# Kernel tuning notes

Hardware: AMD Instinct MI355X
Metric: run time of the kernel (lower is better)

The kernel has to match this reference:

```python
import jax, jax.numpy as jnp
import numpy as np

B, T, NE = 2, 2048, 1024
NH, NKV, HD = 16, 4, 64
GC = 32  # ve_gate_channels
WIN = 1024  # sliding window (left)
EPS = 1e-6


def rope(x, cos, sin):
    # x: (B,T,H,D), cos/sin: (B,T,D//2)
    cos = cos[:, :, None, :]
    sin = sin[:, :, None, :]
    x1, x2 = jnp.split(x, 2, axis=-1)
    return jnp.concatenate([x1 * cos + x2 * sin, -x1 * sin + x2 * cos], axis=-1)


def rmsnorm(x):
    return x * jax.lax.rsqrt(jnp.mean(x * x, axis=-1, keepdims=True) + EPS)


def setup_inputs() -> dict:
    key = jax.random.key(0)
    ks = jax.random.split(key, 7)
    x = jax.random.normal(ks[0], (B, T, NE), jnp.float32)
    ve = jax.random.normal(ks[1], (B, T, NKV * HD), jnp.float32)
    # real RoPE tables (already 'sliced to correct positions')
    inv_freq = 1.0 / (10000.0 ** (jnp.arange(HD // 2, dtype=jnp.float32) / (HD // 2)))
    ang = jnp.arange(T, dtype=jnp.float32)[:, None] * inv_freq[None, :]  # (T, D//2)
    cos = jnp.broadcast_to(jnp.cos(ang)[None], (B, T, HD // 2))
    sin = jnp.broadcast_to(jnp.sin(ang)[None], (B, T, HD // 2))
    s = 0.02
    Wq = jax.random.normal(ks[2], (NE, NH * HD), jnp.float32) * s
    Wk = jax.random.normal(ks[3], (NE, NKV * HD), jnp.float32) * s
    Wv = jax.random.normal(ks[4], (NE, NKV * HD), jnp.float32) * s
    Wo = jax.random.normal(ks[5], (NE, NE), jnp.float32) * s
    Wg = jax.random.normal(ks[6], (GC, NKV), jnp.float32) * s
    return {"x": x, "ve": ve, "cos": cos, "sin": sin,
            "Wq": Wq, "Wk": Wk, "Wv": Wv, "Wo": Wo, "Wg": Wg,
            "window_size": WIN}


def reference(x, ve, cos, sin, Wq, Wk, Wv, Wo, Wg, window_size):
    Bs, Ts, _ = x.shape
    q = (x @ Wq).reshape(Bs, Ts, NH, HD)
    k = (x @ Wk).reshape(Bs, Ts, NKV, HD)
    v = (x @ Wv).reshape(Bs, Ts, NKV, HD)
    # gated value embeddings
    gate = 2.0 * jax.nn.sigmoid(x[..., :GC] @ Wg)  # (B,T,NKV)
    v = v + gate[..., None] * ve.reshape(Bs, Ts, NKV, HD)
    q = rmsnorm(rope(q, cos, sin))
    k = rmsnorm(rope(k, cos, sin))
    # GQA: head h uses kv head h // rep
    rep = NH // NKV
    k = jnp.repeat(k, rep, axis=2)
    v = jnp.repeat(v, rep, axis=2)
    scale = 1.0 / jnp.sqrt(jnp.float32(HD))
    scores = jnp.einsum('bthd,bshd->bhts', q, k) * scale  # (B,H,T,T)
    i = jnp.arange(Ts)[:, None]
    j = jnp.arange(Ts)[None, :]
    mask = (j <= i) & (i - j <= window_size)  # causal + sliding window
    scores = jnp.where(mask, scores, -jnp.inf)
    p = jax.nn.softmax(scores, axis=-1)
    y = jnp.einsum('bhts,bshd->bthd', p, v).reshape(Bs, Ts, NE)
    return y @ Wo
```

## Files before the change

kernel.cpp:

```cpp
#include <hip/hip_runtime.h>
#include <hip/hip_bf16.h>
#include <string.h>

typedef __attribute__((ext_vector_type(8))) short bf16x8;
typedef __attribute__((ext_vector_type(4))) short bf16x4;
typedef __attribute__((ext_vector_type(4))) float f32x4;
typedef __attribute__((ext_vector_type(4))) int i32x4;
typedef __attribute__((ext_vector_type(2))) int i32x2;

#define DEV __device__ __forceinline__
#define WIN_ 1024

DEV short f2bf(float f) {
  __hip_bfloat16 h = __float2bfloat16(f);
  short s; __builtin_memcpy(&s, &h, 2); return s;
}
DEV float bf2f(short s) {
  union { unsigned u; float f; } a; a.u = ((unsigned)(unsigned short)s) << 16;
  return a.f;
}
DEV unsigned pkbf2(float a, float b) {
  __hip_bfloat162 h = __float22bfloat162_rn(make_float2(a, b));
  unsigned u; __builtin_memcpy(&u, &h, 4); return u;
}
DEV float fexp2(float x) {
#if __has_builtin(__builtin_amdgcn_exp2f)
  return __builtin_amdgcn_exp2f(x);
#else
  return exp2f(x);
#endif
}

DEV f32x4 mfma16(bf16x4 a, bf16x4 b, f32x4 c) {
#if __has_builtin(__builtin_amdgcn_mfma_f32_16x16x16bf16_1k)
  return __builtin_amdgcn_mfma_f32_16x16x16bf16_1k(a, b, c, 0, 0, 0);
#else
  asm volatile("s_nop 1\n\tv_mfma_f32_16x16x16_bf16 %0, %1, %2, %0\n\ts_nop 7\n\ts_nop 7"
               : "+v"(c) : "v"(a), "v"(b));
  return c;
#endif
}

DEV void gload16(const short* g, short* l) {
  __builtin_amdgcn_global_load_lds((const __attribute__((address_space(1))) unsigned int*)g,
                                   (__attribute__((address_space(3))) unsigned int*)l,
                                   16, 0, 0);
}

__global__ __launch_bounds__(256) void k_prep(const float* __restrict__ x,
    const float* __restrict__ Wq, const float* __restrict__ Wk, const float* __restrict__ Wv,
    const float* __restrict__ Wo, short* __restrict__ xb, short* __restrict__ WbT,
    short* __restrict__ WoT) {
  const int bid = blockIdx.x;
  if (bid < 4096) {
    int i = bid * 256 + threadIdx.x;
    f32x4 v = *(const f32x4*)(x + (size_t)i * 4);
    i32x2 o = {(int)pkbf2(v[0], v[1]), (int)pkbf2(v[2], v[3])};
    *(i32x2*)(xb + (size_t)i * 4) = o;
    return;
  }
  int t = bid - 4096;
  const float* src; short* dst; int srcld, bx, by;
  if (t < 1024)      { src = Wq; dst = WbT;                        srcld = 1024; bx = t & 31;          by = t >> 5; }
  else if (t < 1280) { src = Wk; dst = WbT + (size_t)1024 * 1024;  srcld = 256;  bx = (t - 1024) & 7;  by = (t - 1024) >> 3; }
  else if (t < 1536) { src = Wv; dst = WbT + (size_t)1280 * 1024;  srcld = 256;  bx = (t - 1280) & 7;  by = (t - 1280) >> 3; }
  else               { src = Wo; dst = WoT;                        srcld = 1024; bx = (t - 1536) & 31; by = (t - 1536) >> 5; }
  __shared__ float tile[32][33];
  const int n0 = bx * 32, k0 = by * 32;
  const int tx = threadIdx.x & 31, ty = threadIdx.x >> 5;
#pragma unroll
  for (int i = 0; i < 4; ++i)
    tile[ty * 4 + i][tx] = src[(size_t)(k0 + ty * 4 + i) * srcld + n0 + tx];
  __syncthreads();
#pragma unroll
  for (int i = 0; i < 4; ++i)
    dst[(size_t)(n0 + ty * 4 + i) * 1024 + k0 + tx] = f2bf(tile[tx][ty * 4 + i]);
}

template <int LDC, bool F32OUT>
__global__ __launch_bounds__(256) void k_gemm_bt(const short* __restrict__ A, const short* __restrict__ BT,
                                                 void* __restrict__ Cv, int K) {
  __shared__ short As[2][8192];
  __shared__ short Bs[2][4096];
  const int tid = threadIdx.x;
  const int l = tid & 63, w = tid >> 6;
  const int l15 = l & 15, hi = l >> 4;
  const int m0 = blockIdx.y * 128, n0 = blockIdx.x * 64;
  const int srow = tid >> 3;
  const int segsw = 8 * ((tid & 7) ^ (srow & 7));
  const int lo = tid * 8;
  const short* pa = A + (size_t)(m0 + srow) * K + segsw;
  const short* pb = BT + (size_t)(n0 + srow) * K + segsw;
  const int f8 = l15 & 7;

  f32x4 acc[2][4];
#pragma unroll
  for (int i = 0; i < 2; ++i)
#pragma unroll
    for (int j = 0; j < 4; ++j) acc[i][j] = (f32x4){0.f, 0.f, 0.f, 0.f};

  auto stage = [&](int buf, int koff) {
    gload16(pa + koff,              &As[buf][lo]);
    gload16(pa + 32 * K + koff,     &As[buf][lo + 2048]);
    gload16(pa + 64 * K + koff,     &As[buf][lo + 4096]);
    gload16(pa + 96 * K + koff,     &As[buf][lo + 6144]);
    gload16(pb + koff,              &Bs[buf][lo]);
    gload16(pb + 32 * K + koff,     &Bs[buf][lo + 2048]);
  };

  stage(0, 0);
  __syncthreads();
  int cur = 0;
  for (int k0 = 0; k0 < K; k0 += 64) {
    if (k0 + 64 < K) stage(cur ^ 1, k0 + 64);
    bf16x8 af[2][2], bfr[4][2];
#pragma unroll
    for (int c = 0; c < 2; ++c) {
      int seg = 8 * ((4 * c + hi) ^ f8);
#pragma unroll
      for (int mi = 0; mi < 2; ++mi)
        af[mi][c] = *(const bf16x8*)&As[cur][(32 * w + 16 * mi + l15) * 64 + seg];
#pragma unroll
      for (int ni = 0; ni < 4; ++ni)
        bfr[ni][c] = *(const bf16x8*)&Bs[cur][(16 * ni + l15) * 64 + seg];
    }
#pragma unroll
    for (int c = 0; c < 2; ++c)
#pragma unroll
      for (int mi = 0; mi < 2; ++mi)
#pragma unroll
        for (int ni = 0; ni < 4; ++ni)
          acc[mi][ni] = __builtin_amdgcn_mfma_f32_16x16x32_bf16(af[mi][c], bfr[ni][c], acc[mi][ni], 0, 0, 0);
    __syncthreads();
    cur ^= 1;
  }
#pragma unroll
  for (int mi = 0; mi < 2; ++mi)
#pragma unroll
    for (int ni = 0; ni < 4; ++ni)
#pragma unroll
      for (int r = 0; r < 4; ++r) {
        int crow = m0 + 32 * w + 16 * mi + 4 * hi + r;
        int ccol = n0 + 16 * ni + l15;
        if (F32OUT) ((float*)Cv)[(size_t)crow * LDC + ccol] = acc[mi][ni][r];
        else        ((short*)Cv)[(size_t)crow * LDC + ccol] = f2bf(acc[mi][ni][r]);
      }
}

__global__ __launch_bounds__(256) void k_post(const short* __restrict__ qkv, const float* __restrict__ x,
    const float* __restrict__ ve, const float* __restrict__ cosp, const float* __restrict__ sinp,
    const float* __restrict__ Wg, short* __restrict__ qh, short* __restrict__ kh, short* __restrict__ vhT) {
  int g = blockIdx.x * 256 + threadIdx.x;
  int hidx = g >> 12;
  int bt = g & 4095;
  int b = bt >> 11, t = bt & 2047;
  const short* rowp = qkv + (size_t)bt * 1536;
  if (hidx < 20) {
    int col0 = (hidx < 16) ? hidx * 64 : 1024 + (hidx - 16) * 64;
    short vals[64];
#pragma unroll
    for (int s8 = 0; s8 < 8; ++s8) *(i32x4*)&vals[s8 * 8] = *(const i32x4*)(rowp + col0 + s8 * 8);
    const float* cp = cosp + (size_t)bt * 32;
    const float* sp = sinp + (size_t)bt * 32;
    float o[64]; float ss = 0.f;
#pragma unroll
    for (int j = 0; j < 32; ++j) {
      float a = bf2f(vals[j]), b2 = bf2f(vals[j + 32]);
      float c = cp[j], s = sp[j];
      float o1 = a * c + b2 * s;
      float o2 = b2 * c - a * s;
      o[j] = o1; o[j + 32] = o2;
      ss += o1 * o1 + o2 * o2;
    }
    float rinv = rsqrtf(ss * (1.f / 64.f) + 1e-6f);
    if (hidx < 16) rinv *= 0.18033688011112042f;
    short* dst = (hidx < 16)
        ? qh + ((size_t)(b * 16 + hidx) * 2048 + t) * 64
        : kh + ((size_t)(b * 4 + (hidx - 16)) * 2048 + t) * 64;
#pragma unroll
    for (int s8 = 0; s8 < 8; ++s8) {
      i32x4 pk;
#pragma unroll
      for (int p = 0; p < 4; ++p) {
        int j = s8 * 8 + p * 2;
        pk[p] = (int)pkbf2(o[j] * rinv, o[j + 1] * rinv);
      }
      *(i32x4*)(dst + s8 * 8) = pk;
    }
  } else {
    int kvh = hidx - 20;
    const float* xr = x + (size_t)bt * 1024;
    float z = 0.f;
#pragma unroll
    for (int gg = 0; gg < 32; ++gg) z += xr[gg] * Wg[gg * 4 + kvh];
    float gate = 2.f / (1.f + __expf(-z));
    const float* vep = ve + (size_t)bt * 256 + kvh * 64;
    short vals[64];
#pragma unroll
    for (int s8 = 0; s8 < 8; ++s8)
      *(i32x4*)&vals[s8 * 8] = *(const i32x4*)(rowp + 1280 + kvh * 64 + s8 * 8);
    short* dst = vhT + (size_t)(b * 4 + kvh) * 64 * 2048 + t;
#pragma unroll
    for (int j = 0; j < 64; ++j) {
      float vv = bf2f(vals[j]) + gate * vep[j];
      dst[(size_t)j * 2048] = f2bf(vv);
    }
  }
}

__global__ __launch_bounds__(256) void k_attn(const short* __restrict__ qh, const short* __restrict__ kh,
                                              const short* __restrict__ vhT, short* __restrict__ yb) {
  __shared__ i32x4 lds4[2][1024];
  char* base = (char*)lds4;
  const int bid = blockIdx.x;
  const int kq = bid >> 8, low = bid & 255;
  const int h = low & 15, b = (low >> 4) & 1, q0 = low >> 5;
  const int qt = (kq == 0) ? (31 - q0) : (kq == 1) ? (16 + q0) : (kq == 2) ? (15 - q0) : q0;
  const int kvh = h >> 2;
  const int qs = qt * 64;
  const int tid = threadIdx.x;
  const int w = tid >> 6, l = tid & 63, l15 = l & 15, hi = l >> 4;
  const int qi = qs + 16 * w + l15;
  const int rsw = (l15 & 7) << 4;

  const short* qb = qh + ((size_t)((b * 16 + h) * 2048 + qs + 16 * w + l15)) * 64;
  bf16x8 qf0 = *(const bf16x8*)(qb + 8 * hi);
  bf16x8 qf1 = *(const bf16x8*)(qb + 32 + 8 * hi);

  f32x4 oacc[4];
#pragma unroll
  for (int i = 0; i < 4; ++i) oacc[i] = (f32x4){0.f, 0.f, 0.f, 0.f};
  float lsum = 0.f;

  const int kt_lo = (qs >= 1024) ? ((qs - 1024) >> 6) : 0;
  const int kt_hi = qs >> 6;
  const short* kbase = kh + ((size_t)(b * 4 + kvh) * 2048) * 64;
  const short* vbase = vhT + ((size_t)(b * 4 + kvh) * 64) * 2048;

  const int srow = tid >> 3, sseg = tid & 7;
  const int swz = (srow & 7) << 4;
  const int ko = ((srow << 7) + (sseg << 4)) ^ swz;
  const short* kp = kbase + (size_t)(kt_lo * 64 + srow) * 64 + sseg * 8;
  const short* vp = vbase + (size_t)srow * 2048 + kt_lo * 64 + sseg * 8;
  i32x4 rk0, rk1, rv0, rv1;

#define LOADT() do { \
    rk0 = *(const i32x4*)kp; \
    rk1 = *(const i32x4*)(kp + 2048); \
    rv0 = *(const i32x4*)vp; \
    rv1 = *(const i32x4*)(vp + 32 * 2048); \
  } while (0)

#define WRITET(DST) do { \
    char* kd = (DST); \
    *(i32x4*)(kd + ko) = rk0; \
    *(i32x4*)(kd + ko + 4096) = rk1; \
    char* vd = kd + 8192; \
    *(i32x4*)(vd + ko) = rv0; \
    *(i32x4*)(vd + ko + 4096) = rv1; \
  } while (0)

  LOADT();
  WRITET(base);
  __syncthreads();

  int cur = 0;

  for (int kt = kt_lo; kt <= kt_hi; ++kt) {
    if (kt < kt_hi) { kp += 4096; vp += 64; LOADT(); }
    char* kbuf = base + cur * 16384;
    char* vbuf = kbuf + 8192;

    __builtin_amdgcn_s_setprio(1);

    f32x4 s[4];
#pragma unroll
    for (int nt = 0; nt < 4; ++nt) s[nt] = (f32x4){0.f, 0.f, 0.f, 0.f};
#pragma unroll
    for (int c = 0; c < 2; ++c) {
      bf16x8 qc = c ? qf1 : qf0;
#pragma unroll
      for (int nt = 0; nt < 4; ++nt) {
        bf16x8 kf = *(const bf16x8*)(kbuf + ((((16 * nt + l15) << 7) + (c << 6) + (hi << 4)) ^ rsw));
        s[nt] = __builtin_amdgcn_mfma_f32_16x16x32_bf16(kf, qc, s[nt], 0, 0, 0);
      }
    }

    if (kt == kt_lo || kt == kt_hi) {
      const int k0 = kt * 64;
#pragma unroll
      for (int nt = 0; nt < 4; ++nt)
#pragma unroll
        for (int r = 0; r < 4; ++r) {
          int kj = k0 + 16 * nt + 4 * hi + r;
          if (kj > qi || (qi - kj) > WIN_) s[nt][r] = -1e30f;
        }
    }

#pragma unroll
    for (int nt = 0; nt < 4; ++nt)
#pragma unroll
      for (int r = 0; r < 4; ++r) s[nt][r] = fexp2(fminf(s[nt][r], 12.5f));
    float r0 = (s[0][0] + s[0][1]) + (s[0][2] + s[0][3]);
    float r1 = (s[1][0] + s[1][1]) + (s[1][2] + s[1][3]);
    float r2 = (s[2][0] + s[2][1]) + (s[2][2] + s[2][3]);
    float r3 = (s[3][0] + s[3][1]) + (s[3][2] + s[3][3]);
    lsum += (r0 + r1) + (r2 + r3);

    bf16x4 pa[4];
#pragma unroll
    for (int nt = 0; nt < 4; ++nt) {
      i32x2 pk = {(int)pkbf2(s[nt][0], s[nt][1]), (int)pkbf2(s[nt][2], s[nt][3])};
      pa[nt] = __builtin_bit_cast(bf16x4, pk);
    }

#pragma unroll
    for (int dt = 0; dt < 4; ++dt) {
      int rowb = ((16 * dt + l15) << 7) + (hi << 3);
#pragma unroll
      for (int nt = 0; nt < 4; ++nt) {
        i32x2 vv = *(const i32x2*)(vbuf + ((rowb + 32 * nt) ^ rsw));
        oacc[dt] = mfma16(__builtin_bit_cast(bf16x4, vv), pa[nt], oacc[dt]);
      }
    }

    __builtin_amdgcn_s_setprio(0);

    if (kt < kt_hi) WRITET(base + (cur ^ 1) * 16384);
    __syncthreads();
    cur ^= 1;
  }
#undef LOADT
#undef WRITET

  lsum += __shfl_xor(lsum, 16);
  lsum += __shfl_xor(lsum, 32);

  float inv = 1.f / lsum;
  size_t orow = (size_t)(b * 2048 + qs + 16 * w + l15);
#pragma unroll
  for (int dt = 0; dt < 4; ++dt) {
    int col0 = h * 64 + 16 * dt + 4 * hi;
    i32x2 pk = {(int)pkbf2(oacc[dt][0] * inv, oacc[dt][1] * inv),
                (int)pkbf2(oacc[dt][2] * inv, oacc[dt][3] * inv)};
    *(i32x2*)(yb + orow * 1024 + col0) = pk;
  }
}

extern "C" void kernel_launch(void* const* d_in, const int* in_sizes, int n_in,
                              void* d_out, int out_size, void* d_ws, size_t ws_size,
                              hipStream_t stream) {
  const float* x    = (const float*)d_in[0];
  const float* ve   = (const float*)d_in[1];
  const float* cosp = (const float*)d_in[2];
  const float* sinp = (const float*)d_in[3];
  const float* Wq   = (const float*)d_in[4];
  const float* Wk   = (const float*)d_in[5];
  const float* Wv   = (const float*)d_in[6];
  const float* Wo   = (const float*)d_in[7];
  const float* Wg   = (const float*)d_in[8];
  float* out = (float*)d_out;

  char* ws = (char*)d_ws;
  short* xb   = (short*)(ws);
  short* WbT  = (short*)(ws + 8388608);
  short* WoT  = (short*)(ws + 11534336);
  short* qkvb = (short*)(ws + 13631488);
  short* qh   = (short*)(ws + 26214400);
  short* kh   = (short*)(ws + 34603008);
  short* vhT  = (short*)(ws + 36700160);
  short* yb   = (short*)(ws + 38797312);

  k_prep<<<6656, 256, 0, stream>>>(x, Wq, Wk, Wv, Wo, xb, WbT, WoT);

  k_gemm_bt<1536, false><<<dim3(24, 32), 256, 0, stream>>>(xb, WbT, qkvb, 1024);

  k_post<<<384, 256, 0, stream>>>(qkvb, x, ve, cosp, sinp, Wg, qh, kh, vhT);

  k_attn<<<1024, 256, 0, stream>>>(qh, kh, vhT, yb);

  k_gemm_bt<1024, true><<<dim3(16, 32), 256, 0, stream>>>(yb, WoT, out, 1024);
}
```

Baseline: 92.07 us.

## Fuse RoPE, RMSNorm and value gating into QKV GEMM epilogue

Removes the separate post-processing kernel and the intermediate bf16 QKV buffer by applying RoPE, RMSNorm, the q scale and the value-embedding gate directly in the QKV GEMM epilogue. Each 64-column tile maps to exactly one head, so the RMS reduction is a 16-lane shuffle across the accumulator fragments. This saves one launch and a round trip of the QKV tensor through global memory. In exchange the epilogue does scattered 2-byte stores and strided transposed V writes, and each block recomputes the gate dot product per row.

```diff
diff --git a/kernel.cpp b/kernel.cpp
--- a/kernel.cpp
+++ b/kernel.cpp
@@ -75,6 +75,119 @@
 #pragma unroll
   for (int i = 0; i < 4; ++i)
     dst[(size_t)(n0 + ty * 4 + i) * 1024 + k0 + tx] = f2bf(tile[tx][ty * 4 + i]);
+}
+
+__global__ __launch_bounds__(256) void k_gemm_qkv(const short* __restrict__ A, const short* __restrict__ BT,
+    const float* __restrict__ x, const float* __restrict__ ve,
+    const float* __restrict__ cosp, const float* __restrict__ sinp, const float* __restrict__ Wg,
+    short* __restrict__ qh, short* __restrict__ kh, short* __restrict__ vhT) {
+  const int K = 1024;
+  __shared__ short As[2][8192];
+  __shared__ short Bs[2][4096];
+  const int tid = threadIdx.x;
+  const int l = tid & 63, w = tid >> 6;
+  const int l15 = l & 15, hi = l >> 4;
+  const int bx = blockIdx.x;
+  const int m0 = blockIdx.y * 128, n0 = bx * 64;
+  const int srow = tid >> 3;
+  const int segsw = 8 * ((tid & 7) ^ (srow & 7));
+  const int lo = tid * 8;
+  const short* pa = A + (size_t)(m0 + srow) * K + segsw;
+  const short* pb = BT + (size_t)(n0 + srow) * K + segsw;
+  const int f8 = l15 & 7;
+
+  f32x4 acc[2][4];
+#pragma unroll
+  for (int i = 0; i < 2; ++i)
+#pragma unroll
+    for (int j = 0; j < 4; ++j) acc[i][j] = (f32x4){0.f, 0.f, 0.f, 0.f};
+
+  auto stage = [&](int buf, int koff) {
+    gload16(pa + koff,          &As[buf][lo]);
+    gload16(pa + 32 * K + koff, &As[buf][lo + 2048]);
+    gload16(pa + 64 * K + koff, &As[buf][lo + 4096]);
+    gload16(pa + 96 * K + koff, &As[buf][lo + 6144]);
+    gload16(pb + koff,          &Bs[buf][lo]);
+    gload16(pb + 32 * K + koff, &Bs[buf][lo + 2048]);
+  };
+
+  stage(0, 0);
+  __syncthreads();
+  int cur = 0;
+  for (int k0 = 0; k0 < K; k0 += 64) {
+    if (k0 + 64 < K) stage(cur ^ 1, k0 + 64);
+    bf16x8 af[2][2], bfr[4][2];
+#pragma unroll
+    for (int c = 0; c < 2; ++c) {
+      int seg = 8 * ((4 * c + hi) ^ f8);
+#pragma unroll
+      for (int mi = 0; mi < 2; ++mi)
+        af[mi][c] = *(const bf16x8*)&As[cur][(32 * w + 16 * mi + l15) * 64 + seg];
+#pragma unroll
+      for (int ni = 0; ni < 4; ++ni)
+        bfr[ni][c] = *(const bf16x8*)&Bs[cur][(16 * ni + l15) * 64 + seg];
+    }
+#pragma unroll
+    for (int c = 0; c < 2; ++c)
+#pragma unroll
+      for (int mi = 0; mi < 2; ++mi)
+#pragma unroll
+        for (int ni = 0; ni < 4; ++ni)
+          acc[mi][ni] = __builtin_amdgcn_mfma_f32_16x16x32_bf16(af[mi][c], bfr[ni][c], acc[mi][ni], 0, 0, 0);
+    __syncthreads();
+    cur ^= 1;
+  }
+
+  if (bx < 20) {
+    short* dst0 = (bx < 16) ? qh : kh;
+#pragma unroll
+    for (int mi = 0; mi < 2; ++mi)
+#pragma unroll
+      for (int r = 0; r < 4; ++r) {
+        int bt = m0 + 32 * w + 16 * mi + 4 * hi + r;
+        int b = bt >> 11, t = bt & 2047;
+        float c0 = cosp[bt * 32 + l15],      s0 = sinp[bt * 32 + l15];
+        float c1 = cosp[bt * 32 + 16 + l15], s1 = sinp[bt * 32 + 16 + l15];
+        float a0 = acc[mi][0][r], b0 = acc[mi][2][r];
+        float a1 = acc[mi][1][r], b1 = acc[mi][3][r];
+        float o0 = a0 * c0 + b0 * s0;
+        float o2 = b0 * c0 - a0 * s0;
+        float o1 = a1 * c1 + b1 * s1;
+        float o3 = b1 * c1 - a1 * s1;
+        float ss = o0 * o0 + o1 * o1 + o2 * o2 + o3 * o3;
+        ss += __shfl_xor(ss, 1); ss += __shfl_xor(ss, 2);
+        ss += __shfl_xor(ss, 4); ss += __shfl_xor(ss, 8);
+        float rinv = rsqrtf(ss * (1.f / 64.f) + 1e-6f);
+        if (bx < 16) rinv *= 0.18033688011112042f;
+        size_t rb = ((size_t)((b * ((bx < 16) ? 16 : 4) + ((bx < 16) ? bx : bx - 16)) * 2048 + t)) * 64;
+        dst0[rb + l15]      = f2bf(o0 * rinv);
+        dst0[rb + 16 + l15] = f2bf(o1 * rinv);
+        dst0[rb + 32 + l15] = f2bf(o2 * rinv);
+        dst0[rb + 48 + l15] = f2bf(o3 * rinv);
+      }
+  } else {
+    const int kvh = bx - 20;
+#pragma unroll
+    for (int mi = 0; mi < 2; ++mi)
+#pragma unroll
+      for (int r = 0; r < 4; ++r) {
+        int bt = m0 + 32 * w + 16 * mi + 4 * hi + r;
+        int b = bt >> 11, t = bt & 2047;
+        const float* xr = x + (size_t)bt * 1024;
+        float z = 0.f;
+#pragma unroll
+        for (int gg = 0; gg < 32; ++gg) z += xr[gg] * Wg[gg * 4 + kvh];
+        float gate = 2.f / (1.f + __expf(-z));
+        const float* vep = ve + (size_t)bt * 256 + kvh * 64;
+        short* dst = vhT + (size_t)(b * 4 + kvh) * 131072 + t;
+#pragma unroll
+        for (int ni = 0; ni < 4; ++ni) {
+          int d = 16 * ni + l15;
+          float vv = acc[mi][ni][r] + gate * vep[d];
+          dst[(size_t)d * 2048] = f2bf(vv);
+        }
+      }
+  }
 }
 
 template <int LDC, bool F32OUT>
@@ -100,12 +213,12 @@
     for (int j = 0; j < 4; ++j) acc[i][j] = (f32x4){0.f, 0.f, 0.f, 0.f};
 
   auto stage = [&](int buf, int koff) {
-    gload16(pa + koff,              &As[buf][lo]);
-    gload16(pa + 32 * K + koff,     &As[buf][lo + 2048]);
-    gload16(pa + 64 * K + koff,     &As[buf][lo + 4096]);
-    gload16(pa + 96 * K + koff,     &As[buf][lo + 6144]);
-    gload16(pb + koff,              &Bs[buf][lo]);
-    gload16(pb + 32 * K + koff,     &Bs[buf][lo + 2048]);
+    gload16(pa + koff,          &As[buf][lo]);
+    gload16(pa + 32 * K + koff, &As[buf][lo + 2048]);
+    gload16(pa + 64 * K + koff, &As[buf][lo + 4096]);
+    gload16(pa + 96 * K + koff, &As[buf][lo + 6144]);
+    gload16(pb + koff,          &Bs[buf][lo]);
+    gload16(pb + 32 * K + koff, &Bs[buf][lo + 2048]);
   };
 
   stage(0, 0);
@@ -145,67 +258,6 @@
         if (F32OUT) ((float*)Cv)[(size_t)crow * LDC + ccol] = acc[mi][ni][r];
         else        ((short*)Cv)[(size_t)crow * LDC + ccol] = f2bf(acc[mi][ni][r]);
       }
-}
-
-__global__ __launch_bounds__(256) void k_post(const short* __restrict__ qkv, const float* __restrict__ x,
-    const float* __restrict__ ve, const float* __restrict__ cosp, const float* __restrict__ sinp,
-    const float* __restrict__ Wg, short* __restrict__ qh, short* __restrict__ kh, short* __restrict__ vhT) {
-  int g = blockIdx.x * 256 + threadIdx.x;
-  int hidx = g >> 12;
-  int bt = g & 4095;
-  int b = bt >> 11, t = bt & 2047;
-  const short* rowp = qkv + (size_t)bt * 1536;
-  if (hidx < 20) {
-    int col0 = (hidx < 16) ? hidx * 64 : 1024 + (hidx - 16) * 64;
-    short vals[64];
-#pragma unroll
-    for (int s8 = 0; s8 < 8; ++s8) *(i32x4*)&vals[s8 * 8] = *(const i32x4*)(rowp + col0 + s8 * 8);
-    const float* cp = cosp + (size_t)bt * 32;
-    const float* sp = sinp + (size_t)bt * 32;
-    float o[64]; float ss = 0.f;
-#pragma unroll
-    for (int j = 0; j < 32; ++j) {
-      float a = bf2f(vals[j]), b2 = bf2f(vals[j + 32]);
-      float c = cp[j], s = sp[j];
-      float o1 = a * c + b2 * s;
-      float o2 = b2 * c - a * s;
-      o[j] = o1; o[j + 32] = o2;
-      ss += o1 * o1 + o2 * o2;
-    }
-    float rinv = rsqrtf(ss * (1.f / 64.f) + 1e-6f);
-    if (hidx < 16) rinv *= 0.18033688011112042f;
-    short* dst = (hidx < 16)
-        ? qh + ((size_t)(b * 16 + hidx) * 2048 + t) * 64
-        : kh + ((size_t)(b * 4 + (hidx - 16)) * 2048 + t) * 64;
-#pragma unroll
-    for (int s8 = 0; s8 < 8; ++s8) {
-      i32x4 pk;
-#pragma unroll
-      for (int p = 0; p < 4; ++p) {
-        int j = s8 * 8 + p * 2;
-        pk[p] = (int)pkbf2(o[j] * rinv, o[j + 1] * rinv);
-      }
-      *(i32x4*)(dst + s8 * 8) = pk;
-    }
-  } else {
-    int kvh = hidx - 20;
-    const float* xr = x + (size_t)bt * 1024;
-    float z = 0.f;
-#pragma unroll
-    for (int gg = 0; gg < 32; ++gg) z += xr[gg] * Wg[gg * 4 + kvh];
-    float gate = 2.f / (1.f + __expf(-z));
-    const float* vep = ve + (size_t)bt * 256 + kvh * 64;
-    short vals[64];
-#pragma unroll
-    for (int s8 = 0; s8 < 8; ++s8)
-      *(i32x4*)&vals[s8 * 8] = *(const i32x4*)(rowp + 1280 + kvh * 64 + s8 * 8);
-    short* dst = vhT + (size_t)(b * 4 + kvh) * 64 * 2048 + t;
-#pragma unroll
-    for (int j = 0; j < 64; ++j) {
-      float vv = bf2f(vals[j]) + gate * vep[j];
-      dst[(size_t)j * 2048] = f2bf(vv);
-    }
-  }
 }
 
 __global__ __launch_bounds__(256) void k_attn(const short* __restrict__ qh, const short* __restrict__ kh,
@@ -365,7 +417,6 @@
   short* xb   = (short*)(ws);
   short* WbT  = (short*)(ws + 8388608);
   short* WoT  = (short*)(ws + 11534336);
-  short* qkvb = (short*)(ws + 13631488);
   short* qh   = (short*)(ws + 26214400);
   short* kh   = (short*)(ws + 34603008);
   short* vhT  = (short*)(ws + 36700160);
@@ -373,9 +424,7 @@
 
   k_prep<<<6656, 256, 0, stream>>>(x, Wq, Wk, Wv, Wo, xb, WbT, WoT);
 
-  k_gemm_bt<1536, false><<<dim3(24, 32), 256, 0, stream>>>(xb, WbT, qkvb, 1024);
-
-  k_post<<<384, 256, 0, stream>>>(qkvb, x, ve, cosp, sinp, Wg, qh, kh, vhT);
+  k_gemm_qkv<<<dim3(24, 32), 256, 0, stream>>>(xb, WbT, x, ve, cosp, sinp, Wg, qh, kh, vhT);
 
   k_attn<<<1024, 256, 0, stream>>>(qh, kh, vhT, yb);
 
```

Result: faster. 85.90 us (-6.7%).
